# Optimization experiments

Hardware: AMD Instinct MI355X
Metric: run time of the kernel (lower is better)

## Reference

```python
import jax, jax.numpy as jnp
import numpy as np

N_NODES = 50000
NEG_SLOPE = 0.2

def _gat_conv(x, W, att_src, att_dst, bias, src, dst):
    # x: [N, in_c] -> h: [N, out_c]
    h = x @ W
    a_src = (h * att_src).sum(-1)  # [N]
    a_dst = (h * att_dst).sum(-1)  # [N]
    e = a_src[src] + a_dst[dst]    # [E]
    e = jnp.where(e > 0, e, NEG_SLOPE * e)  # LeakyReLU
    # segment softmax over destination node neighborhoods
    emax = jax.ops.segment_max(e, dst, num_segments=N_NODES)
    ee = jnp.exp(e - emax[dst])
    denom = jax.ops.segment_sum(ee, dst, num_segments=N_NODES)
    alpha = ee / denom[dst]        # [E]
    out = jax.ops.segment_sum(h[src] * alpha[:, None], dst, num_segments=N_NODES)
    return out + bias

def _with_self_loops(edge_index):
    # PyG GATConv default add_self_loops=True
    loop = jnp.arange(N_NODES, dtype=edge_index.dtype)
    src = jnp.concatenate([edge_index[0], loop])
    dst = jnp.concatenate([edge_index[1], loop])
    return src, dst

def setup_inputs() -> dict:
    key = jax.random.key(0)
    ks = jax.random.split(key, 11)
    in_c, hid_c, out_c = 256, 128, 64
    E = 800000
    x = jax.random.normal(ks[0], (N_NODES, in_c), dtype=jnp.float32)
    edge_index = jax.random.randint(ks[1], (2, E), 0, N_NODES, dtype=jnp.int64)
    s1 = 1.0 / np.sqrt(in_c)
    s2 = 1.0 / np.sqrt(hid_c)
    return {
        "x": x,
        "edge_index": edge_index,
        "W1": jax.random.normal(ks[2], (in_c, hid_c), dtype=jnp.float32) * s1,
        "att_src1": jax.random.normal(ks[3], (hid_c,), dtype=jnp.float32) * s2,
        "att_dst1": jax.random.normal(ks[4], (hid_c,), dtype=jnp.float32) * s2,
        "b1": jax.random.normal(ks[5], (hid_c,), dtype=jnp.float32) * 0.01,
        "W2": jax.random.normal(ks[6], (hid_c, out_c), dtype=jnp.float32) * s2,
        "att_src2": jax.random.normal(ks[7], (out_c,), dtype=jnp.float32) * (1.0 / np.sqrt(out_c)),
        "att_dst2": jax.random.normal(ks[8], (out_c,), dtype=jnp.float32) * (1.0 / np.sqrt(out_c)),
        "b2": jax.random.normal(ks[9], (out_c,), dtype=jnp.float32) * 0.01,
    }

def reference(x, edge_index, W1, att_src1, att_dst1, b1, W2, att_src2, att_dst2, b2):
    src, dst = _with_self_loops(edge_index)
    hid = _gat_conv(x, W1, att_src1, att_dst1, b1, src, dst)
    hid = jax.nn.relu(hid)
    out = _gat_conv(hid, W2, att_src2, att_dst2, b2, src, dst)
    return jax.nn.log_softmax(out, axis=1)
```

## Files before the change

kernel.cpp:

```cpp
#include <hip/hip_runtime.h>
#include <hip/hip_bf16.h>
#include <math.h>

#define N_NODES 50000
#define E_RAW   800000
#define E_TOT   850000
#define NEG_SLOPE 0.2f
#define CAP 64

#define NBKT   392
#define BCAP   2944
#define SCHUNK 4096
#define SB     208

typedef __attribute__((ext_vector_type(8))) short short8;
typedef __attribute__((ext_vector_type(4))) float f32x4;

__device__ __forceinline__ short f2bf(float f) {
    __hip_bfloat16 h = __float2bfloat16(f);
    return *reinterpret_cast<short*>(&h);
}
__device__ __forceinline__ unsigned int f2bfu(float f) {
    __hip_bfloat16 h = __float2bfloat16(f);
    return (unsigned int)*reinterpret_cast<unsigned short*>(&h);
}
__device__ __forceinline__ float bflo(unsigned int u) {
    return __uint_as_float(u << 16);
}
__device__ __forceinline__ float bfhi(unsigned int u) {
    return __uint_as_float(u & 0xffff0000u);
}

template<int K, int N>
__global__ __launch_bounds__(256) void gat_wf_kernel(
        const float* __restrict__ W, short* __restrict__ Wf) {
    constexpr int NT = N / 16;
    const int idx = blockIdx.x * 256 + threadIdx.x;
    if (idx >= K * N) return;
    const int j  = idx & 7;
    const int n  = (idx >> 3) & 15;
    const int q  = (idx >> 7) & 3;
    const int t  = (idx >> 9) % NT;
    const int kc = idx / (512 * NT);
    const int k   = kc * 32 + q * 8 + j;
    const int col = t * 16 + n;
    Wf[idx] = f2bf(W[(size_t)k * N + col]);
}

template<int K, int N, bool BF16_IN>
__device__ __forceinline__ void gemm_att_body(
        const int blk,
        const float* __restrict__ xf, const short* __restrict__ xb,
        const short* __restrict__ Wf,
        const float* __restrict__ att_src, const float* __restrict__ att_dst,
        short* __restrict__ h_bf,
        float* __restrict__ a_src, float* __restrict__ a_dst) {
    constexpr int NT = N / 16;
    constexpr int KC = K / 32;
    const int tid  = threadIdx.x;
    const int lane = tid & 63;
    const int wv   = tid >> 6;
    const int mrow = lane & 15;
    const int q    = lane >> 4;

    const int row0 = blk * 64 + wv * 16;
    const int rowA = row0 + mrow;
    const int rowAc = rowA < N_NODES ? rowA : 0;

    f32x4 acc[NT];
    #pragma unroll
    for (int t = 0; t < NT; ++t) acc[t] = f32x4{0.f, 0.f, 0.f, 0.f};

    #pragma unroll
    for (int kc = 0; kc < KC; ++kc) {
        short8 a;
        if (BF16_IN) {
            a = *(const short8*)&xb[(size_t)rowAc * K + kc * 32 + q * 8];
        } else {
            const float4 f0 = *(const float4*)&xf[(size_t)rowAc * K + kc * 32 + q * 8];
            const float4 f1 = *(const float4*)&xf[(size_t)rowAc * K + kc * 32 + q * 8 + 4];
            a[0] = f2bf(f0.x); a[1] = f2bf(f0.y); a[2] = f2bf(f0.z); a[3] = f2bf(f0.w);
            a[4] = f2bf(f1.x); a[5] = f2bf(f1.y); a[6] = f2bf(f1.z); a[7] = f2bf(f1.w);
        }
        #pragma unroll
        for (int t = 0; t < NT; ++t) {
            const short8 b = *(const short8*)&Wf[((size_t)(kc * NT + t) * 64 + lane) * 8];
            acc[t] = __builtin_amdgcn_mfma_f32_16x16x32_bf16(a, b, acc[t], 0, 0, 0);
        }
    }

    #pragma unroll
    for (int r = 0; r < 4; ++r) {
        const int rowD = row0 + q * 4 + r;
        float ps = 0.0f, pd = 0.0f;
        #pragma unroll
        for (int t = 0; t < NT; ++t) {
            const int col = t * 16 + mrow;
            ps = fmaf(acc[t][r], att_src[col], ps);
            pd = fmaf(acc[t][r], att_dst[col], pd);
        }
        #pragma unroll
        for (int off = 8; off > 0; off >>= 1) {
            ps += __shfl_xor(ps, off);
            pd += __shfl_xor(pd, off);
        }
        if (rowD < N_NODES) {
            if (mrow == 0) { a_src[rowD] = ps; a_dst[rowD] = pd; }
            #pragma unroll
            for (int t = 0; t < NT; ++t)
                h_bf[(size_t)rowD * N + t * 16 + mrow] = f2bf(acc[t][r]);
        }
    }
}

template<int K, int N>
__global__ __launch_bounds__(256) void gat_fat1_kernel(
        const float* __restrict__ xf, const short* __restrict__ Wf,
        const float* __restrict__ att_src, const float* __restrict__ att_dst,
        short* __restrict__ h_bf,
        float* __restrict__ a_src, float* __restrict__ a_dst,
        const int* __restrict__ ei, int* __restrict__ gcnt,
        unsigned int* __restrict__ buf, int GB) {
    __shared__ int hist[NBKT];
    __shared__ int base[NBKT];
    if ((int)blockIdx.x < GB) {
        gemm_att_body<K, N, false>(blockIdx.x, xf, nullptr, Wf,
                                   att_src, att_dst, h_bf, a_src, a_dst);
    } else {
        const int sb = (int)blockIdx.x - GB;
        const int c0 = sb * SCHUNK;
        const int c1 = (c0 + SCHUNK < E_TOT) ? c0 + SCHUNK : E_TOT;
        for (int t = threadIdx.x; t < NBKT; t += 256) hist[t] = 0;
        __syncthreads();
        for (int i = c0 + threadIdx.x; i < c1; i += 256) {
            const int d = (i < E_RAW) ? ei[E_RAW + i] : (i - E_RAW);
            atomicAdd(&hist[d >> 7], 1);
        }
        __syncthreads();
        for (int t = threadIdx.x; t < NBKT; t += 256)
            base[t] = atomicAdd(&gcnt[t], hist[t]);
        __syncthreads();
        for (int t = threadIdx.x; t < NBKT; t += 256) hist[t] = 0;
        __syncthreads();
        for (int i = c0 + threadIdx.x; i < c1; i += 256) {
            int s, d;
            if (i < E_RAW) { s = ei[i]; d = ei[E_RAW + i]; }
            else           { s = d = i - E_RAW; }
            const int b = d >> 7;
            const int p = base[b] + atomicAdd(&hist[b], 1);
            if (p < BCAP)
                buf[(size_t)b * BCAP + p] =
                    ((unsigned int)s << 7) | (unsigned int)(d & 127);
        }
    }
}

__global__ __launch_bounds__(256) void gat_ell_kernel(
        const unsigned int* __restrict__ buf, const int* __restrict__ gcnt,
        int* __restrict__ cnt, unsigned short* __restrict__ srcs) {
    const int b = blockIdx.x;
    __shared__ unsigned int c2[128];
    if (threadIdx.x < 128) c2[threadIdx.x] = 0;
    __syncthreads();
    int n = gcnt[b];
    n = n < BCAP ? n : BCAP;
    const unsigned int* bb = buf + (size_t)b * BCAP;
    for (int i = threadIdx.x; i < n; i += 256) {
        const unsigned int e = bb[i];
        const int dl = (int)(e & 127u);
        const unsigned int s = e >> 7;
        const unsigned int c = atomicAdd(&c2[dl], 1u);
        if (c < CAP)
            srcs[((size_t)((b << 7) + dl) << 6) + c] = (unsigned short)s;
    }
    __syncthreads();
    const int d = (b << 7) + threadIdx.x;
    if (threadIdx.x < 128 && d < N_NODES) {
        unsigned int c = c2[threadIdx.x];
        cnt[d] = (int)(c < CAP ? c : CAP);
    }
}

template<int K, int N, bool BF16_IN>
__global__ __launch_bounds__(256) void gat_gemm_att_kernel(
        const float* __restrict__ xf, const short* __restrict__ xb,
        const short* __restrict__ Wf,
        const float* __restrict__ att_src, const float* __restrict__ att_dst,
        short* __restrict__ h_bf,
        float* __restrict__ a_src, float* __restrict__ a_dst) {
    gemm_att_body<K, N, BF16_IN>(blockIdx.x, xf, xb, Wf,
                                 att_src, att_dst, h_bf, a_src, a_dst);
}

template<int N, bool RELU, bool LSM>
__global__ __launch_bounds__(256) void gat_aggr_kernel(
        const int* __restrict__ cnt, const unsigned short* __restrict__ srcs,
        const float* __restrict__ a_src, const float* __restrict__ a_dst,
        const unsigned short* __restrict__ h_bf, const float* __restrict__ bias,
        float* __restrict__ outf, uint4* __restrict__ outb) {
    constexpr int EPL = N / 16;
    const int lane = threadIdx.x & 63;
    const int wave = threadIdx.x >> 6;
    const int d = blockIdx.x * 4 + wave;
    if (d >= N_NODES) return;
    const int beg = d << 6;
    int deg = cnt[d];
    deg = deg < CAP ? deg : CAP;
    const float ad = a_dst[d];

    const int sreg = (int)srcs[beg + (lane < deg ? lane : 0)];
    float e;
    if (lane < deg) {
        float t = a_src[sreg] + ad;
        e = t > 0.0f ? t : NEG_SLOPE * t;
    } else {
        e = -1e30f;
    }
    float m = e;
    #pragma unroll
    for (int off = 32; off > 0; off >>= 1) m = fmaxf(m, __shfl_xor(m, off));
    const float anum = __expf(e - m);
    float ss = anum;
    #pragma unroll
    for (int off = 32; off > 0; off >>= 1) ss += __shfl_xor(ss, off);
    const float areg = anum / ss;

    const int g   = lane >> 4;
    const int sub = lane & 15;
    float acc[EPL];
    #pragma unroll
    for (int c = 0; c < EPL; ++c) acc[c] = 0.0f;

    const int deg4 = (deg + 3) & ~3;
    int j = 0;
    for (; j + 8 <= deg4; j += 8) {
        const int e0 = j + g;
        const int e1 = j + 4 + g;
        const int s0 = __shfl(sreg, e0);
        const int s1 = __shfl(sreg, e1);
        float al0    = __shfl(areg, e0);
        float al1    = __shfl(areg, e1);
        if (e0 >= deg) al0 = 0.0f;
        if (e1 >= deg) al1 = 0.0f;
        const unsigned short* hp0 = h_bf + (size_t)s0 * N + sub * EPL;
        const unsigned short* hp1 = h_bf + (size_t)s1 * N + sub * EPL;
        if (EPL == 8) {
            const uint4 h0 = *(const uint4*)hp0;
            const uint4 h1 = *(const uint4*)hp1;
            acc[0] = fmaf(al0, bflo(h0.x), acc[0]);
            acc[1] = fmaf(al0, bfhi(h0.x), acc[1]);
            acc[2] = fmaf(al0, bflo(h0.y), acc[2]);
            acc[3] = fmaf(al0, bfhi(h0.y), acc[3]);
            acc[4] = fmaf(al0, bflo(h0.z), acc[4]);
            acc[5] = fmaf(al0, bfhi(h0.z), acc[5]);
            acc[6] = fmaf(al0, bflo(h0.w), acc[6]);
            acc[7] = fmaf(al0, bfhi(h0.w), acc[7]);
            acc[0] = fmaf(al1, bflo(h1.x), acc[0]);
            acc[1] = fmaf(al1, bfhi(h1.x), acc[1]);
            acc[2] = fmaf(al1, bflo(h1.y), acc[2]);
            acc[3] = fmaf(al1, bfhi(h1.y), acc[3]);
            acc[4] = fmaf(al1, bflo(h1.z), acc[4]);
            acc[5] = fmaf(al1, bfhi(h1.z), acc[5]);
            acc[6] = fmaf(al1, bflo(h1.w), acc[6]);
            acc[7] = fmaf(al1, bfhi(h1.w), acc[7]);
        } else {
            const uint2 h0 = *(const uint2*)hp0;
            const uint2 h1 = *(const uint2*)hp1;
            acc[0] = fmaf(al0, bflo(h0.x), acc[0]);
            acc[1] = fmaf(al0, bfhi(h0.x), acc[1]);
            acc[2] = fmaf(al0, bflo(h0.y), acc[2]);
            acc[3] = fmaf(al0, bfhi(h0.y), acc[3]);
            acc[0] = fmaf(al1, bflo(h1.x), acc[0]);
            acc[1] = fmaf(al1, bfhi(h1.x), acc[1]);
            acc[2] = fmaf(al1, bflo(h1.y), acc[2]);
            acc[3] = fmaf(al1, bfhi(h1.y), acc[3]);
        }
    }
    if (j < deg4) {
        const int e0 = j + g;
        const int s0 = __shfl(sreg, e0);
        float al0    = __shfl(areg, e0);
        if (e0 >= deg) al0 = 0.0f;
        const unsigned short* hp0 = h_bf + (size_t)s0 * N + sub * EPL;
        if (EPL == 8) {
            const uint4 h0 = *(const uint4*)hp0;
            acc[0] = fmaf(al0, bflo(h0.x), acc[0]);
            acc[1] = fmaf(al0, bfhi(h0.x), acc[1]);
            acc[2] = fmaf(al0, bflo(h0.y), acc[2]);
            acc[3] = fmaf(al0, bfhi(h0.y), acc[3]);
            acc[4] = fmaf(al0, bflo(h0.z), acc[4]);
            acc[5] = fmaf(al0, bfhi(h0.z), acc[5]);
            acc[6] = fmaf(al0, bflo(h0.w), acc[6]);
            acc[7] = fmaf(al0, bfhi(h0.w), acc[7]);
        } else {
            const uint2 h0 = *(const uint2*)hp0;
            acc[0] = fmaf(al0, bflo(h0.x), acc[0]);
            acc[1] = fmaf(al0, bfhi(h0.x), acc[1]);
            acc[2] = fmaf(al0, bflo(h0.y), acc[2]);
            acc[3] = fmaf(al0, bfhi(h0.y), acc[3]);
        }
    }

    #pragma unroll
    for (int c = 0; c < EPL; ++c) {
        acc[c] += __shfl_xor(acc[c], 16);
        acc[c] += __shfl_xor(acc[c], 32);
    }

    if (LSM) {
        float v[4];
        #pragma unroll
        for (int c = 0; c < 4; ++c) v[c] = acc[c] + bias[sub * 4 + c];
        float mm = fmaxf(fmaxf(v[0], v[1]), fmaxf(v[2], v[3]));
        #pragma unroll
        for (int off = 1; off < 16; off <<= 1) mm = fmaxf(mm, __shfl_xor(mm, off));
        float es = __expf(v[0] - mm) + __expf(v[1] - mm)
                 + __expf(v[2] - mm) + __expf(v[3] - mm);
        #pragma unroll
        for (int off = 1; off < 16; off <<= 1) es += __shfl_xor(es, off);
        const float ls = logf(es);
        if (lane < 16) {
            float4 o;
            o.x = v[0] - mm - ls; o.y = v[1] - mm - ls;
            o.z = v[2] - mm - ls; o.w = v[3] - mm - ls;
            *(float4*)&outf[(size_t)d * N + sub * 4] = o;
        }
    } else {
        if (lane < 16) {
            const float4 b0 = *(const float4*)&bias[sub * 8];
            const float4 b1 = *(const float4*)&bias[sub * 8 + 4];
            float v[8];
            v[0] = acc[0] + b0.x; v[1] = acc[1] + b0.y;
            v[2] = acc[2] + b0.z; v[3] = acc[3] + b0.w;
            v[4] = acc[4] + b1.x; v[5] = acc[5] + b1.y;
            v[6] = acc[6] + b1.z; v[7] = acc[7] + b1.w;
            if (RELU)
                #pragma unroll
                for (int c = 0; c < 8; ++c) v[c] = fmaxf(v[c], 0.0f);
            uint4 p;
            p.x = f2bfu(v[0]) | (f2bfu(v[1]) << 16);
            p.y = f2bfu(v[2]) | (f2bfu(v[3]) << 16);
            p.z = f2bfu(v[4]) | (f2bfu(v[5]) << 16);
            p.w = f2bfu(v[6]) | (f2bfu(v[7]) << 16);
            outb[(size_t)d * (N / 8) + sub] = p;
        }
    }
}

extern "C" void kernel_launch(void* const* d_in, const int* in_sizes, int n_in,
                              void* d_out, int out_size, void* d_ws, size_t ws_size,
                              hipStream_t stream) {
    const float* x        = (const float*)d_in[0];
    const int*   ei       = (const int*)  d_in[1];
    const float* W1       = (const float*)d_in[2];
    const float* att_src1 = (const float*)d_in[3];
    const float* att_dst1 = (const float*)d_in[4];
    const float* b1       = (const float*)d_in[5];
    const float* W2       = (const float*)d_in[6];
    const float* att_src2 = (const float*)d_in[7];
    const float* att_dst2 = (const float*)d_in[8];
    const float* b2       = (const float*)d_in[9];
    float* out = (float*)d_out;
    float* ws  = (float*)d_ws;

    float* a_src1 = ws;
    float* a_dst1 = a_src1 + 50000;
    float* a_src2 = a_dst1 + 50000;
    float* a_dst2 = a_src2 + 50000;
    int*   cnt    = (int*)(a_dst2 + 50000);
    int*   gcnt   = cnt + 50000;
    unsigned int*   buf  = (unsigned int*)(gcnt + 512);
    unsigned short* srcs = (unsigned short*)(buf + (size_t)NBKT * BCAP);
    short* hbf1   = (short*)(srcs + (size_t)N_NODES * CAP);
    short* agg1b  = hbf1  + 6400000;
    short* Wf1    = agg1b + 6400000;
    short* Wf2    = Wf1   + 32768;
    short* hbf2   = hbf1;

    hipMemsetAsync(gcnt, 0, NBKT * sizeof(int), stream);

    const int GB = (N_NODES + 63) / 64;

    gat_wf_kernel<256, 128><<<128, 256, 0, stream>>>(W1, Wf1);
    gat_wf_kernel<128, 64><<<32, 256, 0, stream>>>(W2, Wf2);

    gat_fat1_kernel<256, 128><<<GB + SB, 256, 0, stream>>>(
        x, Wf1, att_src1, att_dst1, hbf1, a_src1, a_dst1,
        ei, gcnt, buf, GB);

    gat_ell_kernel<<<NBKT, 256, 0, stream>>>(buf, gcnt, cnt, srcs);

    gat_aggr_kernel<128, true, false><<<12500, 256, 0, stream>>>(
        cnt, srcs, a_src1, a_dst1, (const unsigned short*)hbf1, b1,
        nullptr, (uint4*)agg1b);

    gat_gemm_att_kernel<128, 64, true><<<GB, 256, 0, stream>>>(
        nullptr, agg1b, Wf2, att_src2, att_dst2, hbf2, a_src2, a_dst2);
    gat_aggr_kernel<64, false, true><<<12500, 256, 0, stream>>>(
        cnt, srcs, a_src2, a_dst2, (const unsigned short*)hbf2, b2,
        out, nullptr);
}
```

Baseline: 220.4 us.

## Map one destination node per 16-lane group in GAT aggregation

Reorganizes the aggregation kernel so each 16-lane quarter-wave handles a whole destination node, giving 16 nodes per block instead of 4. Softmax attention weights and source indices are first computed cooperatively and staged in shared memory, then each group walks its node's edges serially. This removes the cross-group shuffle reduction and the idle lanes at store time, and makes loop trip counts follow each node's actual degree rather than padding. In exchange each group issues its gathers one edge at a time, so there is less memory-level parallelism per node, and the kernel adds two block barriers.

```diff
diff --git a/kernel.cpp b/kernel.cpp
--- a/kernel.cpp
+++ b/kernel.cpp
@@ -15,6 +15,7 @@
 
 typedef __attribute__((ext_vector_type(8))) short short8;
 typedef __attribute__((ext_vector_type(4))) float f32x4;
+typedef __attribute__((ext_vector_type(4))) unsigned short ushort4_t;
 
 __device__ __forceinline__ short f2bf(float f) {
     __hip_bfloat16 h = __float2bfloat16(f);
@@ -199,49 +200,73 @@
         const unsigned short* __restrict__ h_bf, const float* __restrict__ bias,
         float* __restrict__ outf, uint4* __restrict__ outb) {
     constexpr int EPL = N / 16;
-    const int lane = threadIdx.x & 63;
-    const int wave = threadIdx.x >> 6;
-    const int d = blockIdx.x * 4 + wave;
-    if (d >= N_NODES) return;
-    const int beg = d << 6;
-    int deg = cnt[d];
-    deg = deg < CAP ? deg : CAP;
-    const float ad = a_dst[d];
-
-    const int sreg = (int)srcs[beg + (lane < deg ? lane : 0)];
-    float e;
-    if (lane < deg) {
-        float t = a_src[sreg] + ad;
-        e = t > 0.0f ? t : NEG_SLOPE * t;
-    } else {
-        e = -1e30f;
-    }
-    float m = e;
-    #pragma unroll
-    for (int off = 32; off > 0; off >>= 1) m = fmaxf(m, __shfl_xor(m, off));
-    const float anum = __expf(e - m);
-    float ss = anum;
-    #pragma unroll
-    for (int off = 32; off > 0; off >>= 1) ss += __shfl_xor(ss, off);
-    const float areg = anum / ss;
-
-    const int g   = lane >> 4;
-    const int sub = lane & 15;
+    __shared__ __align__(16) float lalpha[1024];
+    __shared__ __align__(8)  unsigned short lsrc[1024];
+    __shared__ int   ldeg[16];
+    __shared__ float ladst[16];
+    const int tid = threadIdx.x;
+    const int d0 = blockIdx.x * 16;
+
+    if (tid < 16) {
+        const int d = d0 + tid;
+        int dg = cnt[d];
+        ldeg[tid]  = dg < CAP ? dg : CAP;
+        ladst[tid] = a_dst[d];
+    }
+    __syncthreads();
+
+    {
+        const int dl = tid >> 4;
+        const int so = (tid & 15) * 4;
+        const int dg = ldeg[dl];
+        const float ad = ladst[dl];
+        const ushort4_t s4 =
+            *(const ushort4_t*)(srcs + ((size_t)(d0 + dl) << 6) + so);
+        float e[4];
+        #pragma unroll
+        for (int i = 0; i < 4; ++i) {
+            if (so + i < dg) {
+                const float t = a_src[(int)s4[i]] + ad;
+                e[i] = t > 0.0f ? t : NEG_SLOPE * t;
+            } else {
+                e[i] = -1e30f;
+            }
+        }
+        float m = fmaxf(fmaxf(e[0], e[1]), fmaxf(e[2], e[3]));
+        #pragma unroll
+        for (int off = 1; off < 16; off <<= 1) m = fmaxf(m, __shfl_xor(m, off));
+        float ex[4], ss = 0.0f;
+        #pragma unroll
+        for (int i = 0; i < 4; ++i) { ex[i] = __expf(e[i] - m); ss += ex[i]; }
+        #pragma unroll
+        for (int off = 1; off < 16; off <<= 1) ss += __shfl_xor(ss, off);
+        const float rinv = 1.0f / ss;
+        float4 av;
+        av.x = ex[0] * rinv; av.y = ex[1] * rinv;
+        av.z = ex[2] * rinv; av.w = ex[3] * rinv;
+        *(float4*)&lalpha[(dl << 6) + so] = av;
+        *(ushort4_t*)&lsrc[(dl << 6) + so] = s4;
+    }
+    __syncthreads();
+
+    const int lane = tid & 63;
+    const int g    = lane >> 4;
+    const int sub  = lane & 15;
+    const int dl   = (tid >> 6) * 4 + g;
+    const int d    = d0 + dl;
+    const int deg  = ldeg[dl];
+    const int base = dl << 6;
+
     float acc[EPL];
     #pragma unroll
     for (int c = 0; c < EPL; ++c) acc[c] = 0.0f;
 
-    const int deg4 = (deg + 3) & ~3;
     int j = 0;
-    for (; j + 8 <= deg4; j += 8) {
-        const int e0 = j + g;
-        const int e1 = j + 4 + g;
-        const int s0 = __shfl(sreg, e0);
-        const int s1 = __shfl(sreg, e1);
-        float al0    = __shfl(areg, e0);
-        float al1    = __shfl(areg, e1);
-        if (e0 >= deg) al0 = 0.0f;
-        if (e1 >= deg) al1 = 0.0f;
+    for (; j + 2 <= deg; j += 2) {
+        const int s0   = (int)lsrc[base + j];
+        const int s1   = (int)lsrc[base + j + 1];
+        const float al0 = lalpha[base + j];
+        const float al1 = lalpha[base + j + 1];
         const unsigned short* hp0 = h_bf + (size_t)s0 * N + sub * EPL;
         const unsigned short* hp1 = h_bf + (size_t)s1 * N + sub * EPL;
         if (EPL == 8) {
@@ -276,11 +301,9 @@
             acc[3] = fmaf(al1, bfhi(h1.y), acc[3]);
         }
     }
-    if (j < deg4) {
-        const int e0 = j + g;
-        const int s0 = __shfl(sreg, e0);
-        float al0    = __shfl(areg, e0);
-        if (e0 >= deg) al0 = 0.0f;
+    if (j < deg) {
+        const int s0    = (int)lsrc[base + j];
+        const float al0 = lalpha[base + j];
         const unsigned short* hp0 = h_bf + (size_t)s0 * N + sub * EPL;
         if (EPL == 8) {
             const uint4 h0 = *(const uint4*)hp0;
@@ -301,12 +324,6 @@
         }
     }
 
-    #pragma unroll
-    for (int c = 0; c < EPL; ++c) {
-        acc[c] += __shfl_xor(acc[c], 16);
-        acc[c] += __shfl_xor(acc[c], 32);
-    }
-
     if (LSM) {
         float v[4];
         #pragma unroll
@@ -319,31 +336,27 @@
         #pragma unroll
         for (int off = 1; off < 16; off <<= 1) es += __shfl_xor(es, off);
         const float ls = logf(es);
-        if (lane < 16) {
-            float4 o;
-            o.x = v[0] - mm - ls; o.y = v[1] - mm - ls;
-            o.z = v[2] - mm - ls; o.w = v[3] - mm - ls;
-            *(float4*)&outf[(size_t)d * N + sub * 4] = o;
-        }
+        float4 o;
+        o.x = v[0] - mm - ls; o.y = v[1] - mm - ls;
+        o.z = v[2] - mm - ls; o.w = v[3] - mm - ls;
+        *(float4*)&outf[(size_t)d * N + sub * 4] = o;
     } else {
-        if (lane < 16) {
-            const float4 b0 = *(const float4*)&bias[sub * 8];
-            const float4 b1 = *(const float4*)&bias[sub * 8 + 4];
-            float v[8];
-            v[0] = acc[0] + b0.x; v[1] = acc[1] + b0.y;
-            v[2] = acc[2] + b0.z; v[3] = acc[3] + b0.w;
-            v[4] = acc[4] + b1.x; v[5] = acc[5] + b1.y;
-            v[6] = acc[6] + b1.z; v[7] = acc[7] + b1.w;
-            if (RELU)
-                #pragma unroll
-                for (int c = 0; c < 8; ++c) v[c] = fmaxf(v[c], 0.0f);
-            uint4 p;
-            p.x = f2bfu(v[0]) | (f2bfu(v[1]) << 16);
-            p.y = f2bfu(v[2]) | (f2bfu(v[3]) << 16);
-            p.z = f2bfu(v[4]) | (f2bfu(v[5]) << 16);
-            p.w = f2bfu(v[6]) | (f2bfu(v[7]) << 16);
-            outb[(size_t)d * (N / 8) + sub] = p;
-        }
+        const float4 b0 = *(const float4*)&bias[sub * 8];
+        const float4 b1 = *(const float4*)&bias[sub * 8 + 4];
+        float v[8];
+        v[0] = acc[0] + b0.x; v[1] = acc[1] + b0.y;
+        v[2] = acc[2] + b0.z; v[3] = acc[3] + b0.w;
+        v[4] = acc[4] + b1.x; v[5] = acc[5] + b1.y;
+        v[6] = acc[6] + b1.z; v[7] = acc[7] + b1.w;
+        if (RELU)
+            #pragma unroll
+            for (int c = 0; c < 8; ++c) v[c] = fmaxf(v[c], 0.0f);
+        uint4 p;
+        p.x = f2bfu(v[0]) | (f2bfu(v[1]) << 16);
+        p.y = f2bfu(v[2]) | (f2bfu(v[3]) << 16);
+        p.z = f2bfu(v[4]) | (f2bfu(v[5]) << 16);
+        p.w = f2bfu(v[6]) | (f2bfu(v[7]) << 16);
+        outb[(size_t)d * (N / 8) + sub] = p;
     }
 }
 
@@ -390,13 +403,13 @@
 
     gat_ell_kernel<<<NBKT, 256, 0, stream>>>(buf, gcnt, cnt, srcs);
 
-    gat_aggr_kernel<128, true, false><<<12500, 256, 0, stream>>>(
+    gat_aggr_kernel<128, true, false><<<3125, 256, 0, stream>>>(
         cnt, srcs, a_src1, a_dst1, (const unsigned short*)hbf1, b1,
         nullptr, (uint4*)agg1b);
 
     gat_gemm_att_kernel<128, 64, true><<<GB, 256, 0, stream>>>(
         nullptr, agg1b, Wf2, att_src2, att_dst2, hbf2, a_src2, a_dst2);
-    gat_aggr_kernel<64, false, true><<<12500, 256, 0, stream>>>(
+    gat_aggr_kernel<64, false, true><<<3125, 256, 0, stream>>>(
         cnt, srcs, a_src2, a_dst2, (const unsigned short*)hbf2, b2,
         out, nullptr);
 }
```

Result: faster. 209.5 us (-4.9%).
